# Kernel tuning notes

Hardware: AMD Instinct MI355X
Metric: run time of the kernel (lower is better)

## Reference

```python
import jax, jax.numpy as jnp
import numpy as np

V, D, K, NH, FF, NV, MC, NL = 4096, 128, 3, 4, 512, 16384, 32, 2
HD = D // NH


def _ln(x, g, b):
    m = x.mean(-1, keepdims=True)
    v = ((x - m) ** 2).mean(-1, keepdims=True)
    return (x - m) / jnp.sqrt(v + 1e-5) * g + b


def setup_inputs() -> dict:
    key = jax.random.key(0)
    ks = iter(jax.random.split(key, 48))
    r = lambda shape, s=1.0: jax.random.normal(next(ks), shape, jnp.float32) * s
    inp = {}
    inp["visits"] = jax.random.randint(next(ks), (NV, MC), 0, V)
    inp["deltas"] = jax.random.uniform(next(ks), (NV,), jnp.float32) * 365.0
    inp["pad_idx"] = 0
    inp["X_hyp"] = r((V, D), 0.03)  # points inside unit Poincare ball
    inp["kernels"] = r((K, V, V), 1.0 / np.sqrt(V))
    inp["proj_W"] = r((K * D, D), 1.0 / np.sqrt(K * D))
    inp["proj_b"] = jnp.zeros((D,), jnp.float32)
    for nm in ["Wq", "Wk", "Wv", "Wo"]:
        inp[nm] = r((NL, D, D), 1.0 / np.sqrt(D))
    for nm in ["bq", "bk", "bv", "bo"]:
        inp[nm] = jnp.zeros((NL, D), jnp.float32)
    inp["ff_W1"] = r((NL, D, FF), 1.0 / np.sqrt(D))
    inp["ff_b1"] = jnp.zeros((NL, FF), jnp.float32)
    inp["ff_W2"] = r((NL, FF, D), 1.0 / np.sqrt(FF))
    inp["ff_b2"] = jnp.zeros((NL, D), jnp.float32)
    inp["ln1_g"] = jnp.ones((NL, D), jnp.float32)
    inp["ln1_b"] = jnp.zeros((NL, D), jnp.float32)
    inp["ln2_g"] = jnp.ones((NL, D), jnp.float32)
    inp["ln2_b"] = jnp.zeros((NL, D), jnp.float32)
    inp["tf_W"] = r((1, D))
    inp["tf_b"] = jnp.zeros((D,), jnp.float32)
    inp["tp_W"] = r((D, D), 1.0 / np.sqrt(D))
    inp["tp_b"] = jnp.zeros((D,), jnp.float32)
    return inp


def reference(visits, deltas, pad_idx, X_hyp, kernels, proj_W, proj_b,
              Wq, Wk, Wv, Wo, bq, bk, bv, bo,
              ff_W1, ff_b1, ff_W2, ff_b2,
              ln1_g, ln1_b, ln2_g, ln2_b,
              tf_W, tf_b, tp_W, tp_b):
    # --- hyperbolic logmap0 (Poincare ball, c=1) ---
    nrm = jnp.clip(jnp.linalg.norm(X_hyp, axis=-1, keepdims=True), 1e-7, 1.0 - 1e-5)
    Z0 = jnp.arctanh(nrm) * X_hyp / nrm  # [V, D]
    # --- multi-scale graph diffusion + projection ---
    Zk = jnp.einsum('kvu,ud->vkd', kernels, Z0).reshape(V, K * D)  # concat over scales
    H = Zk @ proj_W + proj_b  # [V, D]
    # --- global self-attention blocks over all codes (batch 1, L=V) ---
    x = H[None]  # [1, V, D]
    for i in range(NL):
        q = (x @ Wq[i] + bq[i]).reshape(1, V, NH, HD).transpose(0, 2, 1, 3)
        k = (x @ Wk[i] + bk[i]).reshape(1, V, NH, HD).transpose(0, 2, 1, 3)
        v = (x @ Wv[i] + bv[i]).reshape(1, V, NH, HD).transpose(0, 2, 1, 3)
        a = jax.nn.softmax(jnp.einsum('bhqd,bhkd->bhqk', q, k) / np.sqrt(HD), axis=-1)
        o = jnp.einsum('bhqk,bhkd->bhqd', a, v).transpose(0, 2, 1, 3).reshape(1, V, D)
        o = o @ Wo[i] + bo[i]
        x = _ln(x + o, ln1_g[i], ln1_b[i])
        f = jax.nn.gelu(x @ ff_W1[i] + ff_b1[i], approximate=False) @ ff_W2[i] + ff_b2[i]
        x = _ln(x + f, ln2_g[i], ln2_b[i])
    Hr = x[0]  # [V, D]
    # --- time embedding ---
    freq = (deltas[:, None] / 180.0) @ tf_W + tf_b  # [NV, D]
    te = (1.0 - jnp.tanh(freq) ** 2) @ tp_W + tp_b
    # --- ragged per-visit gather + masked mean (the fused-kernel target) ---
    mask = (visits != pad_idx)  # [NV, MC]
    hg = Hr[visits] * mask[..., None]  # [NV, MC, D]
    cnt = mask.sum(-1, keepdims=True)
    vis = hg.sum(1) / jnp.maximum(cnt, 1)  # empty visits -> zeros
    return vis + te
```

## Files before the change

kernel.cpp:

```cpp
#include <hip/hip_runtime.h>


using f16 = _Float16;
typedef f16   f16x8 __attribute__((ext_vector_type(8)));
typedef float f32x4 __attribute__((ext_vector_type(4)));

#define V_   4096
#define D_   128
#define NVIS 16384
#define KS_  8

union H4 { f16 h[4]; uint2 u; };

struct CvtTask { const float* src; void* dst; int R, C, kind; };
struct CvtTasks { CvtTask t[24]; int n; };

__global__ __launch_bounds__(256) void cvt_kernel(CvtTasks T) {
  int tid0 = blockIdx.x * 256 + threadIdx.x;
  int stride = gridDim.x * 256;
  for (int i = 0; i < T.n; i++) {
    CvtTask tk = T.t[i];
    int total = tk.R * tk.C;
    for (int idx = tid0; idx < total; idx += stride) {
      int r = idx / tk.C, c = idx - r * tk.C;
      if (tk.kind == 0)
        ((f16*)tk.dst)[(long long)c * tk.R + r] = (f16)tk.src[idx];
      else
        ((float*)tk.dst)[idx] = tk.src[idx];
    }
  }
}

__global__ __launch_bounds__(256) void logmap_kernel(const float* __restrict__ X, float* __restrict__ Z0) {
  int row = blockIdx.x * 4 + (threadIdx.x >> 6);
  int l = threadIdx.x & 63;
  const float* xr = X + (long long)row * D_;
  float a = xr[l], b = xr[l + 64];
  float ss = a * a + b * b;
  #pragma unroll
  for (int m = 1; m < 64; m <<= 1) ss += __shfl_xor(ss, m);
  float nrm = sqrtf(ss);
  float nc = fminf(fmaxf(nrm, 1e-7f), 1.0f - 1e-5f);
  float scale = atanhf(nc) / nc;
  float* zr = Z0 + (long long)row * D_;
  zr[l] = a * scale; zr[l + 64] = b * scale;
}

struct GemmP {
  const float* A;  long long a_y, a_z;  int lda;
  const f16*  BT;  long long bt_y, bt_z; int ldbt;
  const float* bias; int bias_y, bias_z;
  float* C;  long long c_y, c_z;   int ldc;
  f16*  CH;  long long ch_y, ch_z; int ldch;
  f16*  CHT; long long cht_y, cht_z; int ldcht;
  const float* lng; const float* lnb;
  int K;
};

template<int EPI>
__global__ __launch_bounds__(256) void gemm_kernel(GemmP p) {
  __shared__ alignas(16) f16 As[64][64];
  __shared__ alignas(16) f16 Bs[128][64];
  __shared__ float lnred[2][64][2];
  int tid = threadIdx.x;
  int m0 = blockIdx.x * 64;
  long long by = blockIdx.y, bz = blockIdx.z;
  const float* A = p.A + by * p.a_y + bz * p.a_z + (long long)m0 * p.lda;
  const f16* BT  = p.BT + by * p.bt_y + bz * p.bt_z;

  int wid = tid >> 6, l = tid & 63;
  int lr = l & 15, lg = l >> 4;
  int wm = (wid & 1) * 32;
  int wn = (wid >> 1) * 64;

  f32x4 acc[2][4] = {};

  for (int kb = 0; kb < p.K; kb += 64) {
    __syncthreads();
    #pragma unroll
    for (int pi = 0; pi < 4; pi++) {
      int idx = pi * 256 + tid;
      int r = idx >> 4, c4 = (idx & 15) * 4;
      float4 v = *(const float4*)(A + (long long)r * p.lda + kb + c4);
      int cc = c4 ^ ((r & 7) << 3);
      H4 tmp; tmp.h[0] = (f16)v.x; tmp.h[1] = (f16)v.y; tmp.h[2] = (f16)v.z; tmp.h[3] = (f16)v.w;
      *(uint2*)&As[r][cc] = tmp.u;
    }
    #pragma unroll
    for (int pi = 0; pi < 4; pi++) {
      int idx = pi * 256 + tid;
      int n = idx >> 3, g8 = (idx & 7) * 8;
      f16x8 v = *(const f16x8*)(BT + (long long)n * p.ldbt + kb + g8);
      *(f16x8*)&Bs[n][g8 ^ ((n & 7) << 3)] = v;
    }
    __syncthreads();
    #pragma unroll
    for (int kk = 0; kk < 64; kk += 32) {
      f16x8 a[2], b[4];
      #pragma unroll
      for (int mt = 0; mt < 2; mt++) {
        int r = wm + mt * 16 + lr;
        a[mt] = *(const f16x8*)&As[r][(kk + lg * 8) ^ ((r & 7) << 3)];
      }
      #pragma unroll
      for (int nt = 0; nt < 4; nt++) {
        int n = wn + nt * 16 + lr;
        b[nt] = *(const f16x8*)&Bs[n][(kk + lg * 8) ^ ((n & 7) << 3)];
      }
      #pragma unroll
      for (int mt = 0; mt < 2; mt++)
        #pragma unroll
        for (int nt = 0; nt < 4; nt++)
          acc[mt][nt] = __builtin_amdgcn_mfma_f32_16x16x32_f16(a[mt], b[nt], acc[mt][nt], 0, 0, 0);
    }
  }

  const float* bias = p.bias ? p.bias + by * p.bias_y + bz * p.bias_z : nullptr;

  if constexpr (EPI == 5) {
    float* C = p.C + (long long)m0 * p.ldc;
    #pragma unroll
    for (int nt = 0; nt < 4; nt++) {
      int n = wn + nt * 16 + lr;
      float bv = bias ? bias[n] : 0.0f;
      #pragma unroll
      for (int mt = 0; mt < 2; mt++)
        #pragma unroll
        for (int r = 0; r < 4; r++) {
          int m = wm + mt * 16 + lg * 4 + r;
          acc[mt][nt][r] += bv + C[(long long)m * p.ldc + n];
        }
    }
    #pragma unroll
    for (int mt = 0; mt < 2; mt++)
      #pragma unroll
      for (int r = 0; r < 4; r++) {
        float s = 0.f, ss = 0.f;
        #pragma unroll
        for (int nt = 0; nt < 4; nt++) { float v = acc[mt][nt][r]; s += v; ss += v * v; }
        #pragma unroll
        for (int msk = 1; msk < 16; msk <<= 1) { s += __shfl_xor(s, msk); ss += __shfl_xor(ss, msk); }
        if (lr == 0) {
          int row = wm + mt * 16 + lg * 4 + r;
          lnred[wid >> 1][row][0] = s; lnred[wid >> 1][row][1] = ss;
        }
      }
    __syncthreads();
    #pragma unroll
    for (int mt = 0; mt < 2; mt++)
      #pragma unroll
      for (int r = 0; r < 4; r++) {
        int row = wm + mt * 16 + lg * 4 + r;
        float s  = lnred[0][row][0] + lnred[1][row][0];
        float ss = lnred[0][row][1] + lnred[1][row][1];
        float mean = s * (1.0f / 128.0f);
        float rstd = rsqrtf(ss * (1.0f / 128.0f) - mean * mean + 1e-5f);
        #pragma unroll
        for (int nt = 0; nt < 4; nt++) {
          int n = wn + nt * 16 + lr;
          C[(long long)row * p.ldc + n] = (acc[mt][nt][r] - mean) * rstd * p.lng[n] + p.lnb[n];
        }
      }
    return;
  } else {
    bool do_c  = (EPI == 0 || EPI == 1);
    bool do_h  = (EPI == 4 && bz < 2);
    bool do_ht = (EPI == 3) || (EPI == 4 && bz == 2);
    float* C = nullptr; f16* CH = nullptr; f16* CHT = nullptr;
    if (do_c)  C   = p.C   + by * p.c_y   + bz * p.c_z   + (long long)m0 * p.ldc;
    if (do_h)  CH  = p.CH  + by * p.ch_y  + bz * p.ch_z  + (long long)m0 * p.ldch;
    if (do_ht) CHT = p.CHT + by * p.cht_y + bz * p.cht_z;

    #pragma unroll
    for (int nt = 0; nt < 4; nt++) {
      int n = wn + nt * 16 + lr;
      float bv = bias ? bias[n] : 0.0f;
      #pragma unroll
      for (int mt = 0; mt < 2; mt++) {
        H4 th;
        #pragma unroll
        for (int r = 0; r < 4; r++) {
          float val = acc[mt][nt][r] + bv;
          if (EPI == 1) val = 0.5f * val * (1.0f + erff(val * 0.70710678118654752f));
          int m = wm + mt * 16 + lg * 4 + r;
          if (do_c) C[(long long)m * p.ldc + n] = val;
          if (do_h) CH[(long long)m * p.ldch + n] = (f16)val;
          th.h[r] = (f16)val;
        }
        if (do_ht)
          *(uint2*)&CHT[(long long)n * p.ldcht + m0 + wm + mt * 16 + lg * 4] = th.u;
      }
    }
  }
}

__global__ __launch_bounds__(256) void combine_kernel(const float* __restrict__ Hp, const float* __restrict__ proj_b,
                                                      float* __restrict__ x) {
  int i = blockIdx.x * 256 + threadIdx.x;
  float s = proj_b[i & 127];
  #pragma unroll
  for (int j = 0; j < 12; j++) s += Hp[(long long)j * (V_ * D_) + i];
  x[i] = s;
}

__global__ __launch_bounds__(256) void attn_kernel(const f16* __restrict__ qh, const f16* __restrict__ kh,
                                                   const f16* __restrict__ vT,
                                                   float* __restrict__ Op, float* __restrict__ Ml) {
  __shared__ alignas(16) f16 Ks[64][40];
  __shared__ alignas(16) f16 Vs[32][72];
  __shared__ alignas(16) f16 Ps[4][16][72];
  int tid = threadIdx.x, w = tid >> 6, l = tid & 63, lr = l & 15, lg = l >> 4;
  int h = blockIdx.y, q0 = blockIdx.x * 64, z = blockIdx.z;
  const float sc = 0.17677669529663687f;

  f16x8 aq = *(const f16x8*)&qh[(long long)(q0 + w * 16 + lr) * D_ + h * 32 + lg * 8];
  float mrow = -1e30f, lsum = 0.f;
  f32x4 oacc[2] = {};
  const f32x4 vzero = {0.f, 0.f, 0.f, 0.f};

  for (int kt = z * (V_ / 64 / KS_); kt < (z + 1) * (V_ / 64 / KS_); kt++) {
    int key0 = kt * 64;
    __syncthreads();
    {
      int key = tid >> 2, g8 = (tid & 3) * 8;
      *(f16x8*)&Ks[key][g8] = *(const f16x8*)&kh[(long long)(key0 + key) * D_ + h * 32 + g8];
      int dd = tid >> 3, kg = (tid & 7) * 8;
      *(f16x8*)&Vs[dd][kg] = *(const f16x8*)&vT[(long long)(h * 32 + dd) * V_ + key0 + kg];
    }
    __syncthreads();
    f32x4 st[4];
    #pragma unroll
    for (int t = 0; t < 4; t++) {
      f16x8 bk = *(const f16x8*)&Ks[t * 16 + lr][lg * 8];
      st[t] = __builtin_amdgcn_mfma_f32_16x16x32_f16(bk, aq, vzero, 0, 0, 0);
    }
    float sv[16];
    #pragma unroll
    for (int t = 0; t < 4; t++)
      #pragma unroll
      for (int r = 0; r < 4; r++) sv[t * 4 + r] = st[t][r] * sc;
    float mx = sv[0];
    #pragma unroll
    for (int i = 1; i < 16; i++) mx = fmaxf(mx, sv[i]);
    mx = fmaxf(mx, __shfl_xor(mx, 16));
    mx = fmaxf(mx, __shfl_xor(mx, 32));
    float mn = fmaxf(mrow, mx);
    float alpha = expf(mrow - mn);
    mrow = mn;
    float rs = 0.f, pv[16];
    #pragma unroll
    for (int i = 0; i < 16; i++) { pv[i] = expf(sv[i] - mn); rs += pv[i]; }
    rs += __shfl_xor(rs, 16);
    rs += __shfl_xor(rs, 32);
    lsum = lsum * alpha + rs;
    #pragma unroll
    for (int r = 0; r < 4; r++) {
      float ar = __shfl(alpha, lg * 4 + r);
      oacc[0][r] *= ar; oacc[1][r] *= ar;
    }
    #pragma unroll
    for (int t = 0; t < 4; t++) {
      H4 hh;
      #pragma unroll
      for (int r = 0; r < 4; r++) hh.h[r] = (f16)pv[t * 4 + r];
      *(uint2*)&Ps[w][lr][t * 16 + lg * 4] = hh.u;
    }
    #pragma unroll
    for (int kc = 0; kc < 2; kc++) {
      f16x8 pa = *(const f16x8*)&Ps[w][lr][kc * 32 + lg * 8];
      #pragma unroll
      for (int t = 0; t < 2; t++) {
        f16x8 bvv = *(const f16x8*)&Vs[t * 16 + lr][kc * 32 + lg * 8];
        oacc[t] = __builtin_amdgcn_mfma_f32_16x16x32_f16(pa, bvv, oacc[t], 0, 0, 0);
      }
    }
  }
  #pragma unroll
  for (int t = 0; t < 2; t++)
    #pragma unroll
    for (int r = 0; r < 4; r++) {
      int q = q0 + w * 16 + lg * 4 + r;
      Op[(long long)z * (V_ * D_) + (long long)q * D_ + h * 32 + t * 16 + lr] = oacc[t][r];
    }
  if (l < 16) {
    int q = q0 + w * 16 + l;
    Ml[(z * 4 + h) * V_ + q] = mrow;
    Ml[KS_ * 4 * V_ + (z * 4 + h) * V_ + q] = lsum;
  }
}

__global__ __launch_bounds__(256) void attn_combine(const float* __restrict__ Op, const float* __restrict__ Ml,
                                                    float* __restrict__ o) {
  int i = blockIdx.x * 256 + threadIdx.x;
  int q = i >> 7, h = (i & 127) >> 5;
  float mv[KS_], lv[KS_];
  float m = -1e30f;
  #pragma unroll
  for (int s = 0; s < KS_; s++) {
    mv[s] = Ml[(s * 4 + h) * V_ + q];
    lv[s] = Ml[KS_ * 4 * V_ + (s * 4 + h) * V_ + q];
    m = fmaxf(m, mv[s]);
  }
  float L = 0.f, O = 0.f;
  #pragma unroll
  for (int s = 0; s < KS_; s++) {
    float wgt = expf(mv[s] - m);
    L += wgt * lv[s];
    O += wgt * Op[(long long)s * (V_ * D_) + i];
  }
  o[i] = O / L;
}

__global__ __launch_bounds__(256) void timefeat_kernel(const float* __restrict__ deltas, const float* __restrict__ tf_W,
                                                       const float* __restrict__ tf_b, float* __restrict__ S) {
  int i = blockIdx.x * 256 + threadIdx.x;
  int n = i >> 7, d = i & 127;
  float fr = deltas[n] * (1.0f / 180.0f) * tf_W[d] + tf_b[d];
  float t = tanhf(fr);
  S[i] = 1.0f - t * t;
}

__global__ __launch_bounds__(256) void gather_kernel(const int* __restrict__ visits, const int* __restrict__ pad_ptr,
                                                     const float* __restrict__ Hr, float* __restrict__ out) {
  __shared__ int vis[2][32];
  int tid = threadIdx.x;
  int pad = *pad_ptr;
  int nb = blockIdx.x * 2;
  if (tid < 64) { int s = tid >> 5, c = tid & 31; vis[s][c] = visits[(long long)(nb + s) * 32 + c]; }
  __syncthreads();
  int s = tid >> 7, d = tid & 127;
  float acc = 0.f; int cnt = 0;
  #pragma unroll 8
  for (int c = 0; c < 32; c++) {
    int idx = vis[s][c];
    if (idx != pad) { acc += Hr[(long long)idx * D_ + d]; cnt++; }
  }
  long long oi = (long long)(nb + s) * D_ + d;
  out[oi] += acc / (float)(cnt > 0 ? cnt : 1);
}

extern "C" void kernel_launch(void* const* d_in, const int* in_sizes, int n_in,
                              void* d_out, int out_size, void* d_ws, size_t ws_size,
                              hipStream_t stream) {
  const int*   visits  = (const int*)d_in[0];
  const float* deltas  = (const float*)d_in[1];
  const int*   pad_idx = (const int*)d_in[2];
  const float* X_hyp   = (const float*)d_in[3];
  const float* kernels = (const float*)d_in[4];
  const float* proj_W  = (const float*)d_in[5];
  const float* proj_b  = (const float*)d_in[6];
  const float* Wq = (const float*)d_in[7];
  const float* Wk = (const float*)d_in[8];
  const float* Wv = (const float*)d_in[9];
  const float* Wo = (const float*)d_in[10];
  const float* bq = (const float*)d_in[11];
  const float* bk = (const float*)d_in[12];
  const float* bv = (const float*)d_in[13];
  const float* bo = (const float*)d_in[14];
  const float* ff_W1 = (const float*)d_in[15];
  const float* ff_b1 = (const float*)d_in[16];
  const float* ff_W2 = (const float*)d_in[17];
  const float* ff_b2 = (const float*)d_in[18];
  const float* ln1_g = (const float*)d_in[19];
  const float* ln1_b = (const float*)d_in[20];
  const float* ln2_g = (const float*)d_in[21];
  const float* ln2_b = (const float*)d_in[22];
  const float* tf_W  = (const float*)d_in[23];
  const float* tf_b  = (const float*)d_in[24];
  const float* tp_W  = (const float*)d_in[25];
  const float* tp_b  = (const float*)d_in[26];
  float* out = (float*)d_out;

  char* ws = (char*)d_ws;
  constexpr long long MB = 1ll << 20;
  f16*   projT = (f16*)(ws);
  f16*   qkvT  = (f16*)(ws + 98304);
  f16*   woT   = (f16*)(ws + 294912);
  f16*   w1T   = (f16*)(ws + 360448);
  f16*   w2T   = (f16*)(ws + 622592);
  f16*   tpT   = (f16*)(ws + 884736);
  float* bqkv  = (float*)(ws + 917504);
  float* Z0    = (float*)(ws + 1 * MB);
  f16*   ycatT = (f16*)(ws + 3 * MB);
  float* x     = (float*)(ws + 6 * MB);
  char*  big   = ws + 8 * MB;
  float* Hp    = (float*)big;
  f16*   qk_h  = (f16*)big;
  f16*   vT    = (f16*)(big + 2 * MB);
  float* o_    = (float*)(big + 3 * MB);
  float* Op    = (float*)(big + 7 * MB);
  float* Ml    = (float*)(big + 23 * MB);
  float* t_    = (float*)big;
  float* S_    = (float*)big;
  (void)ws_size; (void)in_sizes; (void)n_in; (void)out_size;

  CvtTasks T; int ntk = 0;
  auto addT = [&](const float* s, void* d, int R, int C, int kind) { T.t[ntk++] = {s, d, R, C, kind}; };
  for (int k = 0; k < 3; k++) addT(proj_W + k * 16384, projT + k * 16384, 128, 128, 0);
  for (int i = 0; i < 2; i++) {
    addT(Wq + i * 16384, qkvT + i * 49152 + 0,     128, 128, 0);
    addT(Wk + i * 16384, qkvT + i * 49152 + 16384, 128, 128, 0);
    addT(Wv + i * 16384, qkvT + i * 49152 + 32768, 128, 128, 0);
    addT(Wo + i * 16384, woT + i * 16384, 128, 128, 0);
    addT(ff_W1 + i * 65536, w1T + i * 65536, 128, 512, 0);
    addT(ff_W2 + i * 65536, w2T + i * 65536, 512, 128, 0);
    addT(bq + i * 128, bqkv + i * 384 + 0,   1, 128, 1);
    addT(bk + i * 128, bqkv + i * 384 + 128, 1, 128, 1);
    addT(bv + i * 128, bqkv + i * 384 + 256, 1, 128, 1);
  }
  addT(tp_W, tpT, 128, 128, 0);
  T.n = ntk;
  cvt_kernel<<<256, 256, 0, stream>>>(T);

  logmap_kernel<<<V_ / 4, 256, 0, stream>>>(X_hyp, Z0);

  {
    GemmP g{};
    g.A = Z0; g.lda = 128;
    g.BT = projT; g.ldbt = 128; g.bt_z = 16384;
    g.CHT = ycatT; g.ldcht = V_; g.cht_z = (long long)128 * V_;
    g.K = 128;
    gemm_kernel<3><<<dim3(64, 1, 3), 256, 0, stream>>>(g);
  }
  {
    GemmP g{};
    g.A = kernels; g.lda = V_; g.a_y = 1024; g.a_z = (long long)V_ * V_;
    g.BT = ycatT;  g.ldbt = V_; g.bt_y = 1024; g.bt_z = (long long)128 * V_;
    g.C = Hp; g.ldc = 128; g.c_y = (long long)V_ * D_; g.c_z = 4ll * V_ * D_;
    g.K = 1024;
    gemm_kernel<0><<<dim3(64, 4, 3), 256, 0, stream>>>(g);
  }
  combine_kernel<<<V_ * D_ / 256, 256, 0, stream>>>(Hp, proj_b, x);

  for (int i = 0; i < 2; i++) {
    {
      GemmP g{};
      g.A = x; g.lda = 128;
      g.BT = qkvT + i * 49152; g.ldbt = 128; g.bt_z = 16384;
      g.bias = bqkv + i * 384; g.bias_z = 128;
      g.CH = qk_h; g.ldch = 128; g.ch_z = (long long)V_ * D_;
      g.CHT = vT; g.ldcht = V_; g.cht_z = 0;
      g.K = 128;
      gemm_kernel<4><<<dim3(64, 1, 3), 256, 0, stream>>>(g);
    }
    attn_kernel<<<dim3(V_ / 64, 4, KS_), 256, 0, stream>>>(qk_h, qk_h + (long long)V_ * D_, vT, Op, Ml);
    attn_combine<<<V_ * D_ / 256, 256, 0, stream>>>(Op, Ml, o_);
    {
      GemmP g{};
      g.A = o_; g.lda = 128;
      g.BT = woT + i * 16384; g.ldbt = 128;
      g.bias = bo + i * 128;
      g.C = x; g.ldc = 128;
      g.lng = ln1_g + i * 128; g.lnb = ln1_b + i * 128;
      g.K = 128;
      gemm_kernel<5><<<dim3(64, 1, 1), 256, 0, stream>>>(g);
    }
    {
      GemmP g{};
      g.A = x; g.lda = 128;
      g.BT = w1T + i * 65536; g.ldbt = 128; g.bt_y = 128 * 128;
      g.bias = ff_b1 + i * 512; g.bias_y = 128;
      g.C = t_; g.ldc = 512; g.c_y = 128;
      g.K = 128;
      gemm_kernel<1><<<dim3(64, 4, 1), 256, 0, stream>>>(g);
    }
    {
      GemmP g{};
      g.A = t_; g.lda = 512;
      g.BT = w2T + i * 65536; g.ldbt = 512;
      g.bias = ff_b2 + i * 128;
      g.C = x; g.ldc = 128;
      g.lng = ln2_g + i * 128; g.lnb = ln2_b + i * 128;
      g.K = 512;
      gemm_kernel<5><<<dim3(64, 1, 1), 256, 0, stream>>>(g);
    }
  }

  timefeat_kernel<<<NVIS * D_ / 256, 256, 0, stream>>>(deltas, tf_W, tf_b, S_);
  {
    GemmP g{};
    g.A = S_; g.lda = 128;
    g.BT = tpT; g.ldbt = 128;
    g.bias = tp_b;
    g.C = out; g.ldc = 128;
    g.K = 128;
    gemm_kernel<0><<<dim3(NVIS / 64, 1, 1), 256, 0, stream>>>(g);
  }
  gather_kernel<<<NVIS / 2, 256, 0, stream>>>(visits, pad_idx, x, out);
}
```

Measured before the change: 640.0 us.

## Fuse prep kernels, attention combine and time features into GEMM prologues; keep fp16 activations

Merges the weight conversion and logmap launches into one prep kernel. Moves the split-K attention combine into the Wo GEMM's A-tile load and the tanh time-feature computation into the time-projection GEMM's A-tile load. LayerNorm epilogues and the combine kernel now also write an fp16 copy of x, and the FFN hidden activation is stored in fp16 only, so later GEMMs load fp16 A tiles directly. This removes several launches and the fp32 round trips of intermediate tensors. In exchange, the Op/Ml reads and the transcendentals are recomputed inside the GEMM load path.

```diff
diff --git a/kernel.cpp b/kernel.cpp
--- a/kernel.cpp
+++ b/kernel.cpp
@@ -13,11 +13,27 @@
 union H4 { f16 h[4]; uint2 u; };
 
 struct CvtTask { const float* src; void* dst; int R, C, kind; };
-struct CvtTasks { CvtTask t[24]; int n; };
-
-__global__ __launch_bounds__(256) void cvt_kernel(CvtTasks T) {
-  int tid0 = blockIdx.x * 256 + threadIdx.x;
-  int stride = gridDim.x * 256;
+struct CvtTasks { CvtTask t[24]; int n; const float* X; float* Z0; };
+
+__global__ __launch_bounds__(256) void prep_kernel(CvtTasks T) {
+  int bid = blockIdx.x;
+  if (bid < V_ / 4) {
+    int row = bid * 4 + (threadIdx.x >> 6);
+    int l = threadIdx.x & 63;
+    const float* xr = T.X + (long long)row * D_;
+    float a = xr[l], b = xr[l + 64];
+    float ss = a * a + b * b;
+    #pragma unroll
+    for (int m = 1; m < 64; m <<= 1) ss += __shfl_xor(ss, m);
+    float nrm = sqrtf(ss);
+    float nc = fminf(fmaxf(nrm, 1e-7f), 1.0f - 1e-5f);
+    float scale = atanhf(nc) / nc;
+    float* zr = T.Z0 + (long long)row * D_;
+    zr[l] = a * scale; zr[l + 64] = b * scale;
+    return;
+  }
+  int tid0 = (bid - V_ / 4) * 256 + threadIdx.x;
+  int stride = 256 * 256;
   for (int i = 0; i < T.n; i++) {
     CvtTask tk = T.t[i];
     int total = tk.R * tk.C;
@@ -31,33 +47,20 @@
   }
 }
 
-__global__ __launch_bounds__(256) void logmap_kernel(const float* __restrict__ X, float* __restrict__ Z0) {
-  int row = blockIdx.x * 4 + (threadIdx.x >> 6);
-  int l = threadIdx.x & 63;
-  const float* xr = X + (long long)row * D_;
-  float a = xr[l], b = xr[l + 64];
-  float ss = a * a + b * b;
-  #pragma unroll
-  for (int m = 1; m < 64; m <<= 1) ss += __shfl_xor(ss, m);
-  float nrm = sqrtf(ss);
-  float nc = fminf(fmaxf(nrm, 1e-7f), 1.0f - 1e-5f);
-  float scale = atanhf(nc) / nc;
-  float* zr = Z0 + (long long)row * D_;
-  zr[l] = a * scale; zr[l + 64] = b * scale;
-}
-
 struct GemmP {
-  const float* A;  long long a_y, a_z;  int lda;
+  const float* A; const f16* AH; long long a_y, a_z; int lda;
   const f16*  BT;  long long bt_y, bt_z; int ldbt;
   const float* bias; int bias_y, bias_z;
   float* C;  long long c_y, c_z;   int ldc;
   f16*  CH;  long long ch_y, ch_z; int ldch;
   f16*  CHT; long long cht_y, cht_z; int ldcht;
   const float* lng; const float* lnb;
+  const float* Op; const float* Ml;
+  const float* deltas; const float* tfW; const float* tfb;
   int K;
 };
 
-template<int EPI>
+template<int EPI, int AMODE>
 __global__ __launch_bounds__(256) void gemm_kernel(GemmP p) {
   __shared__ alignas(16) f16 As[64][64];
   __shared__ alignas(16) f16 Bs[128][64];
@@ -65,8 +68,7 @@
   int tid = threadIdx.x;
   int m0 = blockIdx.x * 64;
   long long by = blockIdx.y, bz = blockIdx.z;
-  const float* A = p.A + by * p.a_y + bz * p.a_z + (long long)m0 * p.lda;
-  const f16* BT  = p.BT + by * p.bt_y + bz * p.bt_z;
+  const f16* BT = p.BT + by * p.bt_y + bz * p.bt_z;
 
   int wid = tid >> 6, l = tid & 63;
   int lr = l & 15, lg = l >> 4;
@@ -77,14 +79,66 @@
 
   for (int kb = 0; kb < p.K; kb += 64) {
     __syncthreads();
-    #pragma unroll
-    for (int pi = 0; pi < 4; pi++) {
-      int idx = pi * 256 + tid;
-      int r = idx >> 4, c4 = (idx & 15) * 4;
-      float4 v = *(const float4*)(A + (long long)r * p.lda + kb + c4);
-      int cc = c4 ^ ((r & 7) << 3);
-      H4 tmp; tmp.h[0] = (f16)v.x; tmp.h[1] = (f16)v.y; tmp.h[2] = (f16)v.z; tmp.h[3] = (f16)v.w;
-      *(uint2*)&As[r][cc] = tmp.u;
+    if constexpr (AMODE == 0) {
+      const float* A = p.A + by * p.a_y + bz * p.a_z + (long long)m0 * p.lda;
+      #pragma unroll
+      for (int pi = 0; pi < 4; pi++) {
+        int idx = pi * 256 + tid;
+        int r = idx >> 4, c4 = (idx & 15) * 4;
+        float4 v = *(const float4*)(A + (long long)r * p.lda + kb + c4);
+        H4 tmp; tmp.h[0] = (f16)v.x; tmp.h[1] = (f16)v.y; tmp.h[2] = (f16)v.z; tmp.h[3] = (f16)v.w;
+        *(uint2*)&As[r][c4 ^ ((r & 7) << 3)] = tmp.u;
+      }
+    } else if constexpr (AMODE == 1) {
+      const f16* AHp = p.AH + by * p.a_y + bz * p.a_z + (long long)m0 * p.lda;
+      #pragma unroll
+      for (int pi = 0; pi < 2; pi++) {
+        int idx = pi * 256 + tid;
+        int r = idx >> 3, g8 = (idx & 7) * 8;
+        f16x8 v = *(const f16x8*)(AHp + (long long)r * p.lda + kb + g8);
+        *(f16x8*)&As[r][g8 ^ ((r & 7) << 3)] = v;
+      }
+    } else if constexpr (AMODE == 2) {
+      #pragma unroll
+      for (int pi = 0; pi < 4; pi++) {
+        int idx = pi * 256 + tid;
+        int r = idx >> 4, c4 = (idx & 15) * 4;
+        int q = m0 + r, d = kb + c4, h = d >> 5;
+        float mv[KS_], m = -1e30f;
+        #pragma unroll
+        for (int s = 0; s < KS_; s++) { mv[s] = p.Ml[(s * 4 + h) * V_ + q]; m = fmaxf(m, mv[s]); }
+        float L = 0.f, wg[KS_];
+        #pragma unroll
+        for (int s = 0; s < KS_; s++) {
+          wg[s] = expf(mv[s] - m);
+          L += wg[s] * p.Ml[KS_ * 4 * V_ + (s * 4 + h) * V_ + q];
+        }
+        float4 av = {0.f, 0.f, 0.f, 0.f};
+        #pragma unroll
+        for (int s = 0; s < KS_; s++) {
+          float4 ov = *(const float4*)&p.Op[(long long)s * (V_ * D_) + (long long)q * D_ + d];
+          av.x += wg[s] * ov.x; av.y += wg[s] * ov.y; av.z += wg[s] * ov.z; av.w += wg[s] * ov.w;
+        }
+        float inv = 1.0f / L;
+        H4 tmp; tmp.h[0] = (f16)(av.x * inv); tmp.h[1] = (f16)(av.y * inv);
+        tmp.h[2] = (f16)(av.z * inv); tmp.h[3] = (f16)(av.w * inv);
+        *(uint2*)&As[r][c4 ^ ((r & 7) << 3)] = tmp.u;
+      }
+    } else {
+      #pragma unroll
+      for (int pi = 0; pi < 4; pi++) {
+        int idx = pi * 256 + tid;
+        int r = idx >> 4, c4 = (idx & 15) * 4;
+        float del = p.deltas[m0 + r] * (1.0f / 180.0f);
+        H4 tmp;
+        #pragma unroll
+        for (int j = 0; j < 4; j++) {
+          float fr = del * p.tfW[kb + c4 + j] + p.tfb[kb + c4 + j];
+          float t = tanhf(fr);
+          tmp.h[j] = (f16)(1.0f - t * t);
+        }
+        *(uint2*)&As[r][c4 ^ ((r & 7) << 3)] = tmp.u;
+      }
     }
     #pragma unroll
     for (int pi = 0; pi < 4; pi++) {
@@ -119,6 +173,7 @@
 
   if constexpr (EPI == 5) {
     float* C = p.C + (long long)m0 * p.ldc;
+    f16* CH = p.CH + (long long)m0 * p.ldch;
     #pragma unroll
     for (int nt = 0; nt < 4; nt++) {
       int n = wn + nt * 16 + lr;
@@ -158,13 +213,15 @@
         #pragma unroll
         for (int nt = 0; nt < 4; nt++) {
           int n = wn + nt * 16 + lr;
-          C[(long long)row * p.ldc + n] = (acc[mt][nt][r] - mean) * rstd * p.lng[n] + p.lnb[n];
+          float val = (acc[mt][nt][r] - mean) * rstd * p.lng[n] + p.lnb[n];
+          C[(long long)row * p.ldc + n] = val;
+          CH[(long long)row * p.ldch + n] = (f16)val;
         }
       }
     return;
   } else {
-    bool do_c  = (EPI == 0 || EPI == 1);
-    bool do_h  = (EPI == 4 && bz < 2);
+    constexpr bool do_c  = (EPI == 0);
+    bool do_h  = (EPI == 1) || (EPI == 4 && bz < 2);
     bool do_ht = (EPI == 3) || (EPI == 4 && bz == 2);
     float* C = nullptr; f16* CH = nullptr; f16* CHT = nullptr;
     if (do_c)  C   = p.C   + by * p.c_y   + bz * p.c_z   + (long long)m0 * p.ldc;
@@ -195,12 +252,13 @@
 }
 
 __global__ __launch_bounds__(256) void combine_kernel(const float* __restrict__ Hp, const float* __restrict__ proj_b,
-                                                      float* __restrict__ x) {
+                                                      float* __restrict__ x, f16* __restrict__ xh) {
   int i = blockIdx.x * 256 + threadIdx.x;
   float s = proj_b[i & 127];
   #pragma unroll
   for (int j = 0; j < 12; j++) s += Hp[(long long)j * (V_ * D_) + i];
   x[i] = s;
+  xh[i] = (f16)s;
 }
 
 __global__ __launch_bounds__(256) void attn_kernel(const f16* __restrict__ qh, const f16* __restrict__ kh,
@@ -287,37 +345,6 @@
     Ml[(z * 4 + h) * V_ + q] = mrow;
     Ml[KS_ * 4 * V_ + (z * 4 + h) * V_ + q] = lsum;
   }
-}
-
-__global__ __launch_bounds__(256) void attn_combine(const float* __restrict__ Op, const float* __restrict__ Ml,
-                                                    float* __restrict__ o) {
-  int i = blockIdx.x * 256 + threadIdx.x;
-  int q = i >> 7, h = (i & 127) >> 5;
-  float mv[KS_], lv[KS_];
-  float m = -1e30f;
-  #pragma unroll
-  for (int s = 0; s < KS_; s++) {
-    mv[s] = Ml[(s * 4 + h) * V_ + q];
-    lv[s] = Ml[KS_ * 4 * V_ + (s * 4 + h) * V_ + q];
-    m = fmaxf(m, mv[s]);
-  }
-  float L = 0.f, O = 0.f;
-  #pragma unroll
-  for (int s = 0; s < KS_; s++) {
-    float wgt = expf(mv[s] - m);
-    L += wgt * lv[s];
-    O += wgt * Op[(long long)s * (V_ * D_) + i];
-  }
-  o[i] = O / L;
-}
-
-__global__ __launch_bounds__(256) void timefeat_kernel(const float* __restrict__ deltas, const float* __restrict__ tf_W,
-                                                       const float* __restrict__ tf_b, float* __restrict__ S) {
-  int i = blockIdx.x * 256 + threadIdx.x;
-  int n = i >> 7, d = i & 127;
-  float fr = deltas[n] * (1.0f / 180.0f) * tf_W[d] + tf_b[d];
-  float t = tanhf(fr);
-  S[i] = 1.0f - t * t;
 }
 
 __global__ __launch_bounds__(256) void gather_kernel(const int* __restrict__ visits, const int* __restrict__ pad_ptr,
@@ -381,18 +408,18 @@
   f16*   tpT   = (f16*)(ws + 884736);
   float* bqkv  = (float*)(ws + 917504);
   float* Z0    = (float*)(ws + 1 * MB);
+  f16*   xh    = (f16*)(ws + 3 * MB);
   f16*   ycatT = (f16*)(ws + 3 * MB);
   float* x     = (float*)(ws + 6 * MB);
   char*  big   = ws + 8 * MB;
   float* Hp    = (float*)big;
   f16*   qk_h  = (f16*)big;
   f16*   vT    = (f16*)(big + 2 * MB);
-  float* o_    = (float*)(big + 3 * MB);
+  f16*   t_h   = (f16*)(big + 3 * MB);
   float* Op    = (float*)(big + 7 * MB);
   float* Ml    = (float*)(big + 23 * MB);
-  float* t_    = (float*)big;
-  float* S_    = (float*)big;
   (void)ws_size; (void)in_sizes; (void)n_in; (void)out_size;
+
 
   CvtTasks T; int ntk = 0;
   auto addT = [&](const float* s, void* d, int R, int C, int kind) { T.t[ntk++] = {s, d, R, C, kind}; };
@@ -409,10 +436,8 @@
     addT(bv + i * 128, bqkv + i * 384 + 256, 1, 128, 1);
   }
   addT(tp_W, tpT, 128, 128, 0);
-  T.n = ntk;
-  cvt_kernel<<<256, 256, 0, stream>>>(T);
-
-  logmap_kernel<<<V_ / 4, 256, 0, stream>>>(X_hyp, Z0);
+  T.n = ntk; T.X = X_hyp; T.Z0 = Z0;
+  prep_kernel<<<V_ / 4 + 256, 256, 0, stream>>>(T);
 
   {
     GemmP g{};
@@ -420,7 +445,7 @@
     g.BT = projT; g.ldbt = 128; g.bt_z = 16384;
     g.CHT = ycatT; g.ldcht = V_; g.cht_z = (long long)128 * V_;
     g.K = 128;
-    gemm_kernel<3><<<dim3(64, 1, 3), 256, 0, stream>>>(g);
+    gemm_kernel<3, 0><<<dim3(64, 1, 3), 256, 0, stream>>>(g);
   }
   {
     GemmP g{};
@@ -428,63 +453,63 @@
     g.BT = ycatT;  g.ldbt = V_; g.bt_y = 1024; g.bt_z = (long long)128 * V_;
     g.C = Hp; g.ldc = 128; g.c_y = (long long)V_ * D_; g.c_z = 4ll * V_ * D_;
     g.K = 1024;
-    gemm_kernel<0><<<dim3(64, 4, 3), 256, 0, stream>>>(g);
-  }
-  combine_kernel<<<V_ * D_ / 256, 256, 0, stream>>>(Hp, proj_b, x);
+    gemm_kernel<0, 0><<<dim3(64, 4, 3), 256, 0, stream>>>(g);
+  }
+  combine_kernel<<<V_ * D_ / 256, 256, 0, stream>>>(Hp, proj_b, x, xh);
 
   for (int i = 0; i < 2; i++) {
     {
       GemmP g{};
-      g.A = x; g.lda = 128;
+      g.AH = xh; g.lda = 128;
       g.BT = qkvT + i * 49152; g.ldbt = 128; g.bt_z = 16384;
       g.bias = bqkv + i * 384; g.bias_z = 128;
       g.CH = qk_h; g.ldch = 128; g.ch_z = (long long)V_ * D_;
       g.CHT = vT; g.ldcht = V_; g.cht_z = 0;
       g.K = 128;
-      gemm_kernel<4><<<dim3(64, 1, 3), 256, 0, stream>>>(g);
+      gemm_kernel<4, 1><<<dim3(64, 1, 3), 256, 0, stream>>>(g);
     }
     attn_kernel<<<dim3(V_ / 64, 4, KS_), 256, 0, stream>>>(qk_h, qk_h + (long long)V_ * D_, vT, Op, Ml);
-    attn_combine<<<V_ * D_ / 256, 256, 0, stream>>>(Op, Ml, o_);
     {
       GemmP g{};
-      g.A = o_; g.lda = 128;
+      g.Op = Op; g.Ml = Ml;
       g.BT = woT + i * 16384; g.ldbt = 128;
       g.bias = bo + i * 128;
       g.C = x; g.ldc = 128;
+      g.CH = xh; g.ldch = 128;
       g.lng = ln1_g + i * 128; g.lnb = ln1_b + i * 128;
       g.K = 128;
-      gemm_kernel<5><<<dim3(64, 1, 1), 256, 0, stream>>>(g);
+      gemm_kernel<5, 2><<<dim3(64, 1, 1), 256, 0, stream>>>(g);
     }
     {
       GemmP g{};
-      g.A = x; g.lda = 128;
+      g.AH = xh; g.lda = 128;
       g.BT = w1T + i * 65536; g.ldbt = 128; g.bt_y = 128 * 128;
       g.bias = ff_b1 + i * 512; g.bias_y = 128;
-      g.C = t_; g.ldc = 512; g.c_y = 128;
+      g.CH = t_h; g.ldch = 512; g.ch_y = 128;
       g.K = 128;
-      gemm_kernel<1><<<dim3(64, 4, 1), 256, 0, stream>>>(g);
+      gemm_kernel<1, 1><<<dim3(64, 4, 1), 256, 0, stream>>>(g);
     }
     {
       GemmP g{};
-      g.A = t_; g.lda = 512;
+      g.AH = t_h; g.lda = 512;
       g.BT = w2T + i * 65536; g.ldbt = 512;
       g.bias = ff_b2 + i * 128;
       g.C = x; g.ldc = 128;
+      g.CH = xh; g.ldch = 128;
       g.lng = ln2_g + i * 128; g.lnb = ln2_b + i * 128;
       g.K = 512;
-      gemm_kernel<5><<<dim3(64, 1, 1), 256, 0, stream>>>(g);
-    }
-  }
-
-  timefeat_kernel<<<NVIS * D_ / 256, 256, 0, stream>>>(deltas, tf_W, tf_b, S_);
+      gemm_kernel<5, 1><<<dim3(64, 1, 1), 256, 0, stream>>>(g);
+    }
+  }
+
   {
     GemmP g{};
-    g.A = S_; g.lda = 128;
+    g.deltas = deltas; g.tfW = tf_W; g.tfb = tf_b;
     g.BT = tpT; g.ldbt = 128;
     g.bias = tp_b;
     g.C = out; g.ldc = 128;
     g.K = 128;
-    gemm_kernel<0><<<dim3(NVIS / 64, 1, 1), 256, 0, stream>>>(g);
+    gemm_kernel<0, 3><<<dim3(NVIS / 64, 1, 1), 256, 0, stream>>>(g);
   }
   gather_kernel<<<NVIS / 2, 256, 0, stream>>>(visits, pad_idx, x, out);
 }
```

Result: slower. 675.7 us (+5.6%).
